# Kernel optimization log

Hardware: AMD Instinct MI355X
Metric: run time of the kernel (lower is better)

Reference implementation:

```python
import jax, jax.numpy as jnp
import numpy as np

B, K, N, D, H, DOUT = 16, 8, 196, 768, 3072, 768


def setup_inputs() -> dict:
    key = jax.random.key(0)
    ks = jax.random.split(key, 5)
    scale_w1 = 1.0 / np.sqrt(D)
    scale_w2 = 1.0 / np.sqrt(H)
    return {
        "slots": jax.random.normal(ks[0], (B, K, D), dtype=jnp.float32),
        "pos_embed": jax.random.normal(ks[1], (N, D), dtype=jnp.float32) * 0.02,
        "map_alpha": jax.random.normal(ks[2], (N, DOUT), dtype=jnp.float32) * 0.02,
        "W1": jax.random.normal(ks[3], (D, H), dtype=jnp.float32) * scale_w1,
        "b1": jnp.zeros((H,), dtype=jnp.float32),
        "W2": jax.random.normal(ks[4], (H, DOUT), dtype=jnp.float32) * scale_w2,
        "b2": jnp.zeros((DOUT,), dtype=jnp.float32),
    }


def reference(slots, pos_embed, map_alpha, W1, b1, W2, b2):
    b, k, d = slots.shape
    n = pos_embed.shape[0]
    # broadcast slots over patches and add positional embedding: (B,K,N,D)
    tokens = slots[:, :, None, :] + pos_embed[None, None, :, :]
    # 2-layer MLP with ReLU
    h = jax.nn.relu(jnp.einsum('bknd,dh->bknh', tokens, W1) + b1)
    y_k = jnp.einsum('bknh,ho->bkno', h, W2) + b2  # (B,K,N,DOUT)
    # softmax over K of map_alpha expanded over (B,K); identical across K -> uniform 1/K,
    # computed explicitly for faithfulness to the original module
    m_k = jax.nn.softmax(jnp.broadcast_to(map_alpha[None, None, :, :], (b, k, n, map_alpha.shape[1])), axis=1)
    y = jnp.einsum('bknd,bknd->bnd', y_k, m_k)
    return y
```

## Files before the change

kernel.cpp:

```cpp
#include <hip/hip_runtime.h>
#include <hip/hip_bf16.h>
#include <stdint.h>


typedef __attribute__((ext_vector_type(8))) short bf16x8;
typedef __attribute__((ext_vector_type(4))) float f32x4;

#define AS1 __attribute__((address_space(1)))
#define AS3 __attribute__((address_space(3)))

#define WAIT_VM(N) asm volatile("s_waitcnt vmcnt(" #N ")" ::: "memory")
#define BAR()      asm volatile("s_barrier" ::: "memory")
#define BAR_LDS()  asm volatile("s_waitcnt lgkmcnt(0)\ns_barrier" ::: "memory")

static __device__ __forceinline__ void gld_lds16(const void* g, void* l) {
    __builtin_amdgcn_global_load_lds((const AS1 unsigned int*)g,
                                     (AS3 unsigned int*)l, 16, 0, 0);
}

static __device__ __forceinline__ unsigned short f2bf(float f) {
    union { float f; unsigned int u; } v; v.f = f;
    unsigned int u = v.u;
    return (unsigned short)((u + 0x7fffu + ((u >> 16) & 1u)) >> 16);
}

__global__ void k_prep(const float* __restrict__ W1, unsigned short* __restrict__ W1t,
                       const float* __restrict__ S, const float* __restrict__ P,
                       unsigned short* __restrict__ A1) {
    int idx = blockIdx.x * blockDim.x + threadIdx.x;
    const int C1n = 96 * 3072;
    const int PKn = 96 * 384;
    if (idx < C1n) {
        int r  = idx % 3072;
        int kc = idx / 3072;
        unsigned int po[4];
        #pragma unroll
        for (int j = 0; j < 4; ++j) {
            unsigned short lo = f2bf(W1[(size_t)(kc * 8 + 2 * j) * 3072 + r]);
            unsigned short hi = f2bf(W1[(size_t)(kc * 8 + 2 * j + 1) * 3072 + r]);
            po[j] = (unsigned int)lo | ((unsigned int)hi << 16);
        }
        size_t dst = ((size_t)(r >> 6) * 12 + (kc >> 3)) * 4096
                   + (size_t)((kc & 7) * 64 + (r & 63)) * 8;
        *(uint4*)(W1t + dst) = make_uint4(po[0], po[1], po[2], po[3]);
    } else if (idx < C1n + PKn) {
        int t = idx - C1n;
        int r  = t % 384;
        int kc = t / 384;
        uint4 o = make_uint4(0u, 0u, 0u, 0u);
        if (r < 324) {
            const float* src = (r < 128) ? (S + (size_t)r * 768 + kc * 8)
                                         : (P + (size_t)(r - 128) * 768 + kc * 8);
            float4 a = *(const float4*)(src);
            float4 b = *(const float4*)(src + 4);
            o.x = (unsigned int)f2bf(a.x) | ((unsigned int)f2bf(a.y) << 16);
            o.y = (unsigned int)f2bf(a.z) | ((unsigned int)f2bf(a.w) << 16);
            o.z = (unsigned int)f2bf(b.x) | ((unsigned int)f2bf(b.y) << 16);
            o.w = (unsigned int)f2bf(b.z) | ((unsigned int)f2bf(b.w) << 16);
        }
        size_t dst = ((size_t)(r >> 6) * 12 + (kc >> 3)) * 4096
                   + (size_t)((kc & 7) * 64 + (r & 63)) * 8;
        *(uint4*)(A1 + dst) = o;
    }
}

__launch_bounds__(256)
__global__ void k_gemm1_w2t(const unsigned short* __restrict__ A,
                            const unsigned short* __restrict__ Bt,
                            float* __restrict__ C,
                            const float* __restrict__ W2,
                            unsigned short* __restrict__ W2t) {
    const int tid = threadIdx.x;
    if (blockIdx.x >= 288) {
        int idx = (blockIdx.x - 288) * 256 + tid;
        int r  = idx % 768;
        int kc = idx / 768;
        unsigned int po[4];
        #pragma unroll
        for (int j = 0; j < 4; ++j) {
            unsigned short lo = f2bf(W2[(size_t)(kc * 8 + 2 * j) * 768 + r]);
            unsigned short hi = f2bf(W2[(size_t)(kc * 8 + 2 * j + 1) * 768 + r]);
            po[j] = (unsigned int)lo | ((unsigned int)hi << 16);
        }
        size_t dst = ((size_t)(r >> 6) * 48 + (kc >> 3)) * 4096
                   + (size_t)((kc & 7) * 64 + (r & 63)) * 8;
        *(uint4*)(W2t + dst) = make_uint4(po[0], po[1], po[2], po[3]);
        return;
    }

    __shared__ unsigned short sm[3 * 8192];
    const int lane = tid & 63;
    const int wave = tid >> 6;
    const int wm = wave >> 1, wn = wave & 1;
    const int q = lane >> 4, l16 = lane & 15;

    const int id = blockIdx.x;
    const int j  = id >> 3;
    const int nt = (id & 7) * 6 + j % 6;
    const int rt = j / 6;

    const unsigned short* Ab = A  + (size_t)rt * 12 * 4096;
    const unsigned short* Bb = Bt + (size_t)nt * 12 * 4096;

    f32x4 acc[2][2] = {};
    const int offA = (wm * 32 + l16) * 8;
    const int offB = 4096 + (wn * 32 + l16) * 8;

    auto stage = [&](int i, unsigned short* d) {
        const unsigned short* Ag = Ab + (size_t)i * 4096;
        const unsigned short* Bg = Bb + (size_t)i * 4096;
        gld_lds16(Ag + tid * 8,        d + tid * 8);
        gld_lds16(Ag + 2048 + tid * 8, d + 2048 + tid * 8);
        gld_lds16(Bg + tid * 8,        d + 4096 + tid * 8);
        gld_lds16(Bg + 2048 + tid * 8, d + 6144 + tid * 8);
    };
    auto compute = [&](const unsigned short* buf) {
        #pragma unroll
        for (int ks = 0; ks < 2; ++ks) {
            const int ko = (ks * 4 + q) * 512;
            bf16x8 af0 = *(const bf16x8*)(buf + ko + offA);
            bf16x8 af1 = *(const bf16x8*)(buf + ko + offA + 128);
            bf16x8 bf0 = *(const bf16x8*)(buf + ko + offB);
            bf16x8 bf1 = *(const bf16x8*)(buf + ko + offB + 128);
            acc[0][0] = __builtin_amdgcn_mfma_f32_16x16x32_bf16(af0, bf0, acc[0][0], 0, 0, 0);
            acc[0][1] = __builtin_amdgcn_mfma_f32_16x16x32_bf16(af0, bf1, acc[0][1], 0, 0, 0);
            acc[1][0] = __builtin_amdgcn_mfma_f32_16x16x32_bf16(af1, bf0, acc[1][0], 0, 0, 0);
            acc[1][1] = __builtin_amdgcn_mfma_f32_16x16x32_bf16(af1, bf1, acc[1][1], 0, 0, 0);
        }
    };

    unsigned short* s0 = sm;
    unsigned short* s1 = sm + 8192;
    unsigned short* s2 = sm + 16384;

    stage(0, s0);
    stage(1, s1);
    for (int i = 0; i < 12; i += 3) {
        stage(i + 2, s2); WAIT_VM(8);
        BAR(); compute(s0); BAR_LDS();
        if (i + 3 < 12) { stage(i + 3, s0); WAIT_VM(8); } else { WAIT_VM(4); }
        BAR(); compute(s1); BAR_LDS();
        if (i + 4 < 12) { stage(i + 4, s1); WAIT_VM(8); }
        else if (i + 3 < 12) { WAIT_VM(4); }
        else { WAIT_VM(0); }
        BAR(); compute(s2);
        if (i + 3 < 12) BAR_LDS();
    }

    const int row0 = rt * 64 + wm * 32;
    const int col0 = nt * 64 + wn * 32;
    #pragma unroll
    for (int ii = 0; ii < 2; ++ii) {
        #pragma unroll
        for (int jj = 0; jj < 2; ++jj) {
            int col = col0 + jj * 16 + l16;
            #pragma unroll
            for (int r = 0; r < 4; ++r) {
                int row = row0 + ii * 16 + q * 4 + r;
                if (row < 324) C[(size_t)row * 3072 + col] = acc[ii][jj][r];
            }
        }
    }
}

__global__ void k_hbar(const float* __restrict__ C1, const float* __restrict__ b1,
                       unsigned short* __restrict__ Hb) {
    const int bid  = blockIdx.x;
    const int tid  = threadIdx.x;
    const int bx   = bid % 50;
    const int yq   = bid / 50;
    const int lane = tid & 63;
    const int wv   = tid >> 6;
    const int hc   = yq * 4 + wv;
    const int h0   = hc * 8;
    int bn = bx * 64 + lane;
    if (bn > 3135) bn = 3135;
    const int b = bn / 196;
    const int n = bn - b * 196;
    const float* prow = C1 + (size_t)(128 + n) * 3072 + h0;
    float4 pA = *(const float4*)(prow);
    float4 pB = *(const float4*)(prow + 4);
    float4 bA = *(const float4*)(b1 + h0);
    float4 bB = *(const float4*)(b1 + h0 + 4);
    float pb[8] = { pA.x + bA.x, pA.y + bA.y, pA.z + bA.z, pA.w + bA.w,
                    pB.x + bB.x, pB.y + bB.y, pB.z + bB.z, pB.w + bB.w };
    float acc[8] = {};
    #pragma unroll
    for (int k = 0; k < 8; ++k) {
        const float* srow = C1 + (size_t)(b * 8 + k) * 3072 + h0;
        float4 sA_ = *(const float4*)(srow);
        float4 sB_ = *(const float4*)(srow + 4);
        acc[0] += fmaxf(sA_.x + pb[0], 0.f);
        acc[1] += fmaxf(sA_.y + pb[1], 0.f);
        acc[2] += fmaxf(sA_.z + pb[2], 0.f);
        acc[3] += fmaxf(sA_.w + pb[3], 0.f);
        acc[4] += fmaxf(sB_.x + pb[4], 0.f);
        acc[5] += fmaxf(sB_.y + pb[5], 0.f);
        acc[6] += fmaxf(sB_.z + pb[6], 0.f);
        acc[7] += fmaxf(sB_.w + pb[7], 0.f);
    }
    unsigned int w0 = (unsigned int)f2bf(acc[0] * 0.125f) | ((unsigned int)f2bf(acc[1] * 0.125f) << 16);
    unsigned int w1 = (unsigned int)f2bf(acc[2] * 0.125f) | ((unsigned int)f2bf(acc[3] * 0.125f) << 16);
    unsigned int w2 = (unsigned int)f2bf(acc[4] * 0.125f) | ((unsigned int)f2bf(acc[5] * 0.125f) << 16);
    unsigned int w3 = (unsigned int)f2bf(acc[6] * 0.125f) | ((unsigned int)f2bf(acc[7] * 0.125f) << 16);
    size_t dst = ((size_t)bx * 48 + (hc >> 3)) * 4096
               + (size_t)((hc & 7) * 64 + lane) * 8;
    *(uint4*)(Hb + dst) = make_uint4(w0, w1, w2, w3);
}

__launch_bounds__(512)
__global__ void k_gemm2(const unsigned short* __restrict__ Hb,
                        const unsigned short* __restrict__ W2t,
                        const float* __restrict__ b2, float* __restrict__ out) {
    __shared__ unsigned short sm[3 * 12288];

    const int tid  = threadIdx.x;
    const int lane = tid & 63;
    const int wave = tid >> 6;
    const int wm = wave >> 1, wn = wave & 1;
    const int q = lane >> 4, l16 = lane & 15;

    const int id = blockIdx.x;
    int rt, nt;
    if (id < 288) { rt = (id / 96) * 8 + (id & 7); nt = (id % 96) >> 3; }
    else          { rt = 24; nt = id - 288; }

    const unsigned short* A0b = Hb  + ((size_t)(2 * rt)     * 48) * 4096;
    const unsigned short* A1b = Hb  + ((size_t)(2 * rt + 1) * 48) * 4096;
    const unsigned short* Bb  = W2t + ((size_t)nt * 48) * 4096;

    f32x4 acc[2][2] = {};

    auto stage = [&](int i, unsigned short* d) {
        gld_lds16(A0b + (size_t)i * 4096 + tid * 8, d + tid * 8);
        gld_lds16(A1b + (size_t)i * 4096 + tid * 8, d + 4096 + tid * 8);
        gld_lds16(Bb  + (size_t)i * 4096 + tid * 8, d + 8192 + tid * 8);
    };

    const int r0 = wm * 32 + l16;
    const int aoff0 = (r0 >> 6) * 4096 + (r0 & 63) * 8;
    const int r1 = wm * 32 + 16 + l16;
    const int aoff1 = (r1 >> 6) * 4096 + (r1 & 63) * 8;
    const int boff  = 8192 + (wn * 32 + l16) * 8;

    auto compute = [&](const unsigned short* buf) {
        #pragma unroll
        for (int ks = 0; ks < 2; ++ks) {
            const int ko = (ks * 4 + q) * 512;
            bf16x8 af0 = *(const bf16x8*)(buf + aoff0 + ko);
            bf16x8 af1 = *(const bf16x8*)(buf + aoff1 + ko);
            bf16x8 bf0 = *(const bf16x8*)(buf + boff + ko);
            bf16x8 bf1 = *(const bf16x8*)(buf + boff + ko + 128);
            acc[0][0] = __builtin_amdgcn_mfma_f32_16x16x32_bf16(af0, bf0, acc[0][0], 0, 0, 0);
            acc[0][1] = __builtin_amdgcn_mfma_f32_16x16x32_bf16(af0, bf1, acc[0][1], 0, 0, 0);
            acc[1][0] = __builtin_amdgcn_mfma_f32_16x16x32_bf16(af1, bf0, acc[1][0], 0, 0, 0);
            acc[1][1] = __builtin_amdgcn_mfma_f32_16x16x32_bf16(af1, bf1, acc[1][1], 0, 0, 0);
        }
    };

    unsigned short* s0 = sm;
    unsigned short* s1 = sm + 12288;
    unsigned short* s2 = sm + 24576;

    stage(0, s0);
    stage(1, s1);
    for (int i = 0; i < 48; i += 3) {
        stage(i + 2, s2); WAIT_VM(6);
        BAR(); compute(s0); BAR_LDS();
        if (i + 3 < 48) { stage(i + 3, s0); WAIT_VM(6); } else { WAIT_VM(3); }
        BAR(); compute(s1); BAR_LDS();
        if (i + 4 < 48) { stage(i + 4, s1); WAIT_VM(6); }
        else if (i + 3 < 48) { WAIT_VM(3); }
        else { WAIT_VM(0); }
        BAR(); compute(s2);
        if (i + 3 < 48) BAR_LDS();
    }

    const int row0 = rt * 128 + wm * 32;
    const int col0 = nt * 64 + wn * 32;
    #pragma unroll
    for (int ii = 0; ii < 2; ++ii) {
        #pragma unroll
        for (int jj = 0; jj < 2; ++jj) {
            int col = col0 + jj * 16 + l16;
            float bv = b2[col];
            #pragma unroll
            for (int r = 0; r < 4; ++r) {
                int row = row0 + ii * 16 + q * 4 + r;
                if (row < 3136) out[(size_t)row * 768 + col] = acc[ii][jj][r] + bv;
            }
        }
    }
}

extern "C" void kernel_launch(void* const* d_in, const int* in_sizes, int n_in,
                              void* d_out, int out_size, void* d_ws, size_t ws_size,
                              hipStream_t stream) {
    const float* slots  = (const float*)d_in[0];
    const float* pos    = (const float*)d_in[1];
    const float* W1     = (const float*)d_in[3];
    const float* b1     = (const float*)d_in[4];
    const float* W2     = (const float*)d_in[5];
    const float* b2     = (const float*)d_in[6];
    float* out = (float*)d_out;

    size_t off = 0;
    auto alloc = [&](size_t bytes) {
        void* p = (char*)d_ws + off;
        off += (bytes + 255) & ~(size_t)255;
        return p;
    };
    unsigned short* W1t = (unsigned short*)alloc((size_t)3072 * 768 * 2);
    unsigned short* W2t = (unsigned short*)alloc((size_t)768 * 3072 * 2);
    unsigned short* A1  = (unsigned short*)alloc((size_t)384 * 768 * 2);
    float*          C1  = (float*)alloc((size_t)384 * 3072 * 4);
    unsigned short* Hb  = (unsigned short*)alloc((size_t)50 * 48 * 4096 * 2);

    k_prep<<<1296, 256, 0, stream>>>(W1, W1t, slots, pos, A1);
    k_gemm1_w2t<<<1440, 256, 0, stream>>>(A1, W1t, C1, W2, W2t);
    k_hbar<<<4800, 256, 0, stream>>>(C1, b1, Hb);
    k_gemm2<<<300, 512, 0, stream>>>(Hb, W2t, b2, out);
}
```

Measured before the change: 128.5 us.

## Use 2 waves per gemm2 block with 64x64 per-wave tiles

Cuts the second GEMM kernel from 8 waves per block to 2 waves, each computing a 64x64 output tile with a 4x4 grid of MFMA accumulators instead of 32x32. Each thread now issues four times as many async global-to-LDS loads per stage, and the vmcnt wait thresholds are scaled to match. The aim is more MFMA work per LDS fragment load and fewer barrier participants. The cost is more registers per thread, fewer waves per block to hide latency, and only 300 blocks of 2 waves to cover the GPU.

Result: slower. 146.7 us (+14.2%).

```diff
diff --git a/kernel.cpp b/kernel.cpp
--- a/kernel.cpp
+++ b/kernel.cpp
@@ -208,7 +208,7 @@
     *(uint4*)(Hb + dst) = make_uint4(w0, w1, w2, w3);
 }
 
-__launch_bounds__(512)
+__launch_bounds__(128)
 __global__ void k_gemm2(const unsigned short* __restrict__ Hb,
                         const unsigned short* __restrict__ W2t,
                         const float* __restrict__ b2, float* __restrict__ out) {
@@ -216,8 +216,7 @@
 
     const int tid  = threadIdx.x;
     const int lane = tid & 63;
-    const int wave = tid >> 6;
-    const int wm = wave >> 1, wn = wave & 1;
+    const int w    = tid >> 6;
     const int q = lane >> 4, l16 = lane & 15;
 
     const int id = blockIdx.x;
@@ -229,32 +228,39 @@
     const unsigned short* A1b = Hb  + ((size_t)(2 * rt + 1) * 48) * 4096;
     const unsigned short* Bb  = W2t + ((size_t)nt * 48) * 4096;
 
-    f32x4 acc[2][2] = {};
+    f32x4 acc[4][4] = {};
 
     auto stage = [&](int i, unsigned short* d) {
-        gld_lds16(A0b + (size_t)i * 4096 + tid * 8, d + tid * 8);
-        gld_lds16(A1b + (size_t)i * 4096 + tid * 8, d + 4096 + tid * 8);
-        gld_lds16(Bb  + (size_t)i * 4096 + tid * 8, d + 8192 + tid * 8);
-    };
-
-    const int r0 = wm * 32 + l16;
-    const int aoff0 = (r0 >> 6) * 4096 + (r0 & 63) * 8;
-    const int r1 = wm * 32 + 16 + l16;
-    const int aoff1 = (r1 >> 6) * 4096 + (r1 & 63) * 8;
-    const int boff  = 8192 + (wn * 32 + l16) * 8;
-
+        const unsigned short* Ag0 = A0b + (size_t)i * 4096;
+        const unsigned short* Ag1 = A1b + (size_t)i * 4096;
+        const unsigned short* Bg  = Bb  + (size_t)i * 4096;
+        #pragma unroll
+        for (int u = 0; u < 4; ++u) {
+            const int c = (u * 128 + tid) * 8;
+            gld_lds16(Ag0 + c, d + c);
+            gld_lds16(Ag1 + c, d + 4096 + c);
+            gld_lds16(Bg  + c, d + 8192 + c);
+        }
+    };
+
+    const int abase = w * 4096;
     auto compute = [&](const unsigned short* buf) {
         #pragma unroll
         for (int ks = 0; ks < 2; ++ks) {
             const int ko = (ks * 4 + q) * 512;
-            bf16x8 af0 = *(const bf16x8*)(buf + aoff0 + ko);
-            bf16x8 af1 = *(const bf16x8*)(buf + aoff1 + ko);
-            bf16x8 bf0 = *(const bf16x8*)(buf + boff + ko);
-            bf16x8 bf1 = *(const bf16x8*)(buf + boff + ko + 128);
-            acc[0][0] = __builtin_amdgcn_mfma_f32_16x16x32_bf16(af0, bf0, acc[0][0], 0, 0, 0);
-            acc[0][1] = __builtin_amdgcn_mfma_f32_16x16x32_bf16(af0, bf1, acc[0][1], 0, 0, 0);
-            acc[1][0] = __builtin_amdgcn_mfma_f32_16x16x32_bf16(af1, bf0, acc[1][0], 0, 0, 0);
-            acc[1][1] = __builtin_amdgcn_mfma_f32_16x16x32_bf16(af1, bf1, acc[1][1], 0, 0, 0);
+            bf16x8 af[4], bfr[4];
+            #pragma unroll
+            for (int ii = 0; ii < 4; ++ii)
+                af[ii] = *(const bf16x8*)(buf + abase + ko + (ii * 16 + l16) * 8);
+            #pragma unroll
+            for (int jj = 0; jj < 4; ++jj)
+                bfr[jj] = *(const bf16x8*)(buf + 8192 + ko + (jj * 16 + l16) * 8);
+            #pragma unroll
+            for (int ii = 0; ii < 4; ++ii)
+                #pragma unroll
+                for (int jj = 0; jj < 4; ++jj)
+                    acc[ii][jj] = __builtin_amdgcn_mfma_f32_16x16x32_bf16(
+                        af[ii], bfr[jj], acc[ii][jj], 0, 0, 0);
         }
     };
 
@@ -265,23 +271,23 @@
     stage(0, s0);
     stage(1, s1);
     for (int i = 0; i < 48; i += 3) {
-        stage(i + 2, s2); WAIT_VM(6);
+        stage(i + 2, s2); WAIT_VM(24);
         BAR(); compute(s0); BAR_LDS();
-        if (i + 3 < 48) { stage(i + 3, s0); WAIT_VM(6); } else { WAIT_VM(3); }
+        if (i + 3 < 48) { stage(i + 3, s0); WAIT_VM(24); } else { WAIT_VM(12); }
         BAR(); compute(s1); BAR_LDS();
-        if (i + 4 < 48) { stage(i + 4, s1); WAIT_VM(6); }
-        else if (i + 3 < 48) { WAIT_VM(3); }
+        if (i + 4 < 48) { stage(i + 4, s1); WAIT_VM(24); }
+        else if (i + 3 < 48) { WAIT_VM(12); }
         else { WAIT_VM(0); }
         BAR(); compute(s2);
         if (i + 3 < 48) BAR_LDS();
     }
 
-    const int row0 = rt * 128 + wm * 32;
-    const int col0 = nt * 64 + wn * 32;
+    const int row0 = rt * 128 + w * 64;
+    const int col0 = nt * 64;
     #pragma unroll
-    for (int ii = 0; ii < 2; ++ii) {
-        #pragma unroll
-        for (int jj = 0; jj < 2; ++jj) {
+    for (int ii = 0; ii < 4; ++ii) {
+        #pragma unroll
+        for (int jj = 0; jj < 4; ++jj) {
             int col = col0 + jj * 16 + l16;
             float bv = b2[col];
             #pragma unroll
@@ -319,5 +325,5 @@
     k_prep<<<1296, 256, 0, stream>>>(W1, W1t, slots, pos, A1);
     k_gemm1_w2t<<<1440, 256, 0, stream>>>(A1, W1t, C1, W2, W2t);
     k_hbar<<<4800, 256, 0, stream>>>(C1, b1, Hb);
-    k_gemm2<<<300, 512, 0, stream>>>(Hb, W2t, b2, out);
-}
+    k_gemm2<<<300, 128, 0, stream>>>(Hb, W2t, b2, out);
+}
```
